# Kernel tuning notes

Measured on AMD Instinct MI355X. Metric: run time of the kernel, lower is better.

Reference implementation:

```python
import jax, jax.numpy as jnp
import numpy as np

N_NODES = 100000
N_EDGES = 1600000
IN_CH = 256
PROJ = 128
HID = 128
OUT = 32


def setup_inputs() -> dict:
    key = jax.random.key(0)
    ks = jax.random.split(key, 16)
    def lin(kw, kb, fan_in, fan_out):
        s = 1.0 / np.sqrt(fan_in)
        W = jax.random.uniform(kw, (fan_in, fan_out), jnp.float32, -s, s)
        b = jax.random.uniform(kb, (fan_out,), jnp.float32, -s, s)
        return W, b
    x = jax.random.normal(ks[0], (N_NODES, IN_CH), jnp.float32)
    edge_index = jax.random.randint(ks[1], (2, N_EDGES), 0, N_NODES, jnp.int32)
    edge_weight = jax.random.uniform(ks[2], (N_EDGES, 1), jnp.float32)
    Wp, bp = lin(ks[3], ks[4], IN_CH, PROJ)
    W1, b1 = lin(ks[5], ks[6], PROJ, HID)
    W2, b2 = lin(ks[7], ks[8], HID, HID)
    Wl1, bl1 = lin(ks[9], ks[10], HID, HID)
    Wl2, bl2 = lin(ks[11], ks[12], HID, OUT)
    return {"x": x, "edge_index": edge_index, "edge_weight": edge_weight,
            "Wp": Wp, "bp": bp, "W1": W1, "b1": b1, "W2": W2, "b2": b2,
            "Wl1": Wl1, "bl1": bl1, "Wl2": Wl2, "bl2": bl2}


def gcn_conv(x, W, b, src, dst, ew, n):
    # PyG GCNConv: add self-loops (weight 1), symmetric normalization.
    deg = jax.ops.segment_sum(ew, dst, num_segments=n) + 1.0  # self-loop adds 1
    dinv = jnp.where(deg > 0, jax.lax.rsqrt(deg), 0.0)        # [N]
    norm = dinv[src] * ew * dinv[dst]                          # [E]
    h = x @ W                                                  # [N, out]
    agg = jax.ops.segment_sum(norm[:, None] * h[src], dst, num_segments=n)
    agg = agg + (dinv * dinv)[:, None] * h                     # self-loop messages
    return agg + b


def reference(x, edge_index, edge_weight, Wp, bp, W1, b1, W2, b2, Wl1, bl1, Wl2, bl2):
    n = x.shape[0]
    src, dst = edge_index[0], edge_index[1]
    ew = edge_weight.squeeze(-1)
    h = jax.nn.relu(x @ Wp + bp)
    h = jax.nn.relu(gcn_conv(h, W1, b1, src, dst, ew, n))
    h = jax.nn.relu(gcn_conv(h, W2, b2, src, dst, ew, n))
    h = jax.nn.relu(h @ Wl1 + bl1)
    logits = h @ Wl2 + bl2
    return jax.nn.softmax(logits, axis=-1)
```

## Files before the change

kernel.cpp:

```cpp
#include <hip/hip_runtime.h>


typedef __attribute__((ext_vector_type(8))) short bf16x8;
typedef __attribute__((ext_vector_type(4))) short bf16x4;
typedef __attribute__((ext_vector_type(4))) float f32x4;

__device__ __forceinline__ void atomAddF(float* p, float v) {
    unsafeAtomicAdd(p, v);
}

__device__ __forceinline__ ushort bf16_rne(float x) {
    unsigned int u = __float_as_uint(x);
    return (ushort)((u + 0x7FFFu + ((u >> 16) & 1u)) >> 16);
}

__device__ __forceinline__ int swz(int row, int k) {
    return k ^ (((row >> 1) & 3) << 3);
}

__global__ void deg_cnt_kernel(const int* __restrict__ dst, const float* __restrict__ ew,
                               unsigned long long* __restrict__ packed, int E) {
    int e = blockIdx.x * blockDim.x + threadIdx.x;
    if (e < E) {
        int d = dst[e];
        unsigned int fx = __float2uint_rn(ew[e] * 16777216.0f);
        atomicAdd(&packed[d], (1ULL << 32) | (unsigned long long)fx);
    }
}

__global__ void dinv_kernel(const unsigned long long* __restrict__ packed,
                            float* __restrict__ dinv, int N) {
    int i = blockIdx.x * blockDim.x + threadIdx.x;
    if (i < N) {
        float deg = (float)(unsigned int)(packed[i] & 0xFFFFFFFFull) * (1.0f / 16777216.0f);
        dinv[i] = 1.0f / sqrtf(deg + 1.0f);
    }
}

__global__ __launch_bounds__(256) void scan_reduce(const unsigned long long* __restrict__ packed,
                                                   int* __restrict__ bsum, int M) {
    __shared__ int wsum[4];
    const int t = threadIdx.x;
    const int base = blockIdx.x * 2048 + t * 8;
    int s = 0;
#pragma unroll
    for (int j = 0; j < 8; j++) {
        int i = base + j;
        if (i < M) s += (int)(packed[i] >> 32);
    }
#pragma unroll
    for (int off = 1; off < 64; off <<= 1) s += __shfl_xor(s, off);
    if ((t & 63) == 0) wsum[t >> 6] = s;
    __syncthreads();
    if (t == 0) bsum[blockIdx.x] = wsum[0] + wsum[1] + wsum[2] + wsum[3];
}

__global__ void scan_bsum(int* __restrict__ bsum, int* __restrict__ rowptr_last, int nb) {
    const int lane = threadIdx.x;
    const int chunk = (nb + 63) / 64;
    const int b0 = lane * chunk;
    const int b1 = min(b0 + chunk, nb);
    int s = 0;
    for (int i = b0; i < b1; i++) s += bsum[i];
    int inc = s;
#pragma unroll
    for (int off = 1; off < 64; off <<= 1) {
        int u = __shfl_up(inc, off);
        if (lane >= off) inc += u;
    }
    int run = inc - s;
    for (int i = b0; i < b1; i++) {
        int v = bsum[i];
        bsum[i] = run;
        run += v;
    }
    if (lane == 63) *rowptr_last = inc;
}

__global__ __launch_bounds__(256) void scan_down(const unsigned long long* __restrict__ packed,
                                                 const int* __restrict__ bsum,
                                                 int* __restrict__ rowptr,
                                                 int* __restrict__ cur, int M) {
    __shared__ int wpre[4];
    const int t = threadIdx.x;
    const int lane = t & 63;
    const int w = t >> 6;
    const int base = blockIdx.x * 2048 + t * 8;
    int c[8];
    int s = 0;
#pragma unroll
    for (int j = 0; j < 8; j++) {
        int i = base + j;
        c[j] = (i < M) ? (int)(packed[i] >> 32) : 0;
        s += c[j];
    }
    int inc = s;
#pragma unroll
    for (int off = 1; off < 64; off <<= 1) {
        int u = __shfl_up(inc, off);
        if (lane >= off) inc += u;
    }
    if (lane == 63) wpre[w] = inc;
    __syncthreads();
    int woff = 0;
#pragma unroll
    for (int i = 0; i < 4; i++)
        if (i < w) woff += wpre[i];
    int run = bsum[blockIdx.x] + woff + (inc - s);
#pragma unroll
    for (int j = 0; j < 8; j++) {
        int i = base + j;
        if (i < M) {
            rowptr[i] = run;
            cur[i] = run;
            run += c[j];
        }
    }
}

__global__ void reorder_kernel(const int* __restrict__ src, const int* __restrict__ dst,
                               const float* __restrict__ ew, const float* __restrict__ dinv,
                               int* __restrict__ cur, int2* __restrict__ pairs, int E) {
    int e = blockIdx.x * blockDim.x + threadIdx.x;
    if (e < E) {
        int s = src[e], d = dst[e];
        float w = dinv[s] * ew[e] * dinv[d];
        int pos = atomicAdd(&cur[d], 1);
        pairs[pos] = make_int2(s, __float_as_int(w));
    }
}

__global__ __launch_bounds__(256) void gather_kernel(
    const int* __restrict__ rowptr, const int2* __restrict__ pairs,
    const float* __restrict__ dinv, const float* __restrict__ hW,
    float* __restrict__ agg, int M)
{
    int gid = blockIdx.x * blockDim.x + threadIdx.x;
    int n = gid >> 5;
    int c = (gid & 31) * 4;
    if (n >= M) return;
    int beg = rowptr[n], end = rowptr[n + 1];
    float di = dinv[n];
    float s = di * di;
    float4 v = *reinterpret_cast<const float4*>(&hW[(size_t)n * 128 + c]);
    float4 acc0 = make_float4(s * v.x, s * v.y, s * v.z, s * v.w);
    float4 acc1 = make_float4(0.f, 0.f, 0.f, 0.f);

    int e = beg;
    for (; e + 4 <= end; e += 4) {
        int2 p0 = pairs[e + 0];
        int2 p1 = pairs[e + 1];
        int2 p2 = pairs[e + 2];
        int2 p3 = pairs[e + 3];
        float4 h0 = *reinterpret_cast<const float4*>(&hW[(size_t)p0.x * 128 + c]);
        float4 h1 = *reinterpret_cast<const float4*>(&hW[(size_t)p1.x * 128 + c]);
        float4 h2 = *reinterpret_cast<const float4*>(&hW[(size_t)p2.x * 128 + c]);
        float4 h3 = *reinterpret_cast<const float4*>(&hW[(size_t)p3.x * 128 + c]);
        float w0 = __int_as_float(p0.y), w1 = __int_as_float(p1.y);
        float w2 = __int_as_float(p2.y), w3 = __int_as_float(p3.y);
        acc0.x = fmaf(w0, h0.x, acc0.x); acc0.y = fmaf(w0, h0.y, acc0.y);
        acc0.z = fmaf(w0, h0.z, acc0.z); acc0.w = fmaf(w0, h0.w, acc0.w);
        acc1.x = fmaf(w1, h1.x, acc1.x); acc1.y = fmaf(w1, h1.y, acc1.y);
        acc1.z = fmaf(w1, h1.z, acc1.z); acc1.w = fmaf(w1, h1.w, acc1.w);
        acc0.x = fmaf(w2, h2.x, acc0.x); acc0.y = fmaf(w2, h2.y, acc0.y);
        acc0.z = fmaf(w2, h2.z, acc0.z); acc0.w = fmaf(w2, h2.w, acc0.w);
        acc1.x = fmaf(w3, h3.x, acc1.x); acc1.y = fmaf(w3, h3.y, acc1.y);
        acc1.z = fmaf(w3, h3.z, acc1.z); acc1.w = fmaf(w3, h3.w, acc1.w);
    }
    for (; e < end; e++) {
        int2 p = pairs[e];
        float w = __int_as_float(p.y);
        float4 h = *reinterpret_cast<const float4*>(&hW[(size_t)p.x * 128 + c]);
        acc0.x = fmaf(w, h.x, acc0.x);
        acc0.y = fmaf(w, h.y, acc0.y);
        acc0.z = fmaf(w, h.z, acc0.z);
        acc0.w = fmaf(w, h.w, acc0.w);
    }
    acc0.x += acc1.x; acc0.y += acc1.y; acc0.z += acc1.z; acc0.w += acc1.w;
    *reinterpret_cast<float4*>(&agg[(size_t)n * 128 + c]) = acc0;
}

template<int K, bool IN_BR, bool OUT_BR>
__global__ __launch_bounds__(256) void gemm_mfma(
    const float* __restrict__ A, const float* __restrict__ W,
    const float* __restrict__ in_bias, const float* __restrict__ out_bias,
    float* __restrict__ C, int M)
{
    __shared__ ushort Ah[128][40], Al[128][40], Bh[128][40], Bl[128][40];

    const int tid = threadIdx.x;
    const int lane = tid & 63;
    const int wave = tid >> 6;
    const int wm = (wave >> 1) * 64;
    const int wn = (wave & 1) * 64;
    const int m0 = blockIdx.x * 128;

    f32x4 acc[4][4] = {};

    const int ar = tid >> 1;
    const int ak = (tid & 1) * 16;
    const int bn = (tid & 31) * 4;
    const int bk = (tid >> 5) * 4;

    const int fm = lane & 15;
    const int fk = (lane >> 4) * 8;

    for (int k0 = 0; k0 < K; k0 += 32) {
        __syncthreads();
        {
            const bool valid = (m0 + ar) < M;
            const float* srcp = &A[(size_t)(m0 + ar) * K + k0 + ak];
#pragma unroll
            for (int q = 0; q < 2; q++) {
                float vv[8];
                if (valid) {
                    *reinterpret_cast<float4*>(&vv[0]) = *reinterpret_cast<const float4*>(srcp + q * 8);
                    *reinterpret_cast<float4*>(&vv[4]) = *reinterpret_cast<const float4*>(srcp + q * 8 + 4);
                } else {
#pragma unroll
                    for (int j = 0; j < 8; j++) vv[j] = 0.f;
                }
                if (IN_BR) {
                    const float* bp_ = &in_bias[k0 + ak + q * 8];
#pragma unroll
                    for (int j = 0; j < 8; j++) vv[j] = fmaxf(vv[j] + bp_[j], 0.f);
                }
#pragma unroll
                for (int h = 0; h < 2; h++) {
                    ushort hh[4], ll[4];
#pragma unroll
                    for (int j = 0; j < 4; j++) {
                        float x = vv[h * 4 + j];
                        ushort hi = bf16_rne(x);
                        float fhi = __uint_as_float((unsigned int)hi << 16);
                        hh[j] = hi;
                        ll[j] = bf16_rne(x - fhi);
                    }
                    int col = swz(ar, ak + q * 8 + h * 4);
                    *reinterpret_cast<bf16x4*>(&Ah[ar][col]) = *reinterpret_cast<bf16x4*>(hh);
                    *reinterpret_cast<bf16x4*>(&Al[ar][col]) = *reinterpret_cast<bf16x4*>(ll);
                }
            }
        }
        {
            float rr[4][4];
#pragma unroll
            for (int i = 0; i < 4; i++)
                *reinterpret_cast<float4*>(rr[i]) =
                    *reinterpret_cast<const float4*>(&W[(size_t)(k0 + bk + i) * 128 + bn]);
#pragma unroll
            for (int j = 0; j < 4; j++) {
                ushort hh[4], ll[4];
#pragma unroll
                for (int i = 0; i < 4; i++) {
                    float x = rr[i][j];
                    ushort hi = bf16_rne(x);
                    float fhi = __uint_as_float((unsigned int)hi << 16);
                    hh[i] = hi;
                    ll[i] = bf16_rne(x - fhi);
                }
                int n = bn + j;
                int col = swz(n, bk);
                *reinterpret_cast<bf16x4*>(&Bh[n][col]) = *reinterpret_cast<bf16x4*>(hh);
                *reinterpret_cast<bf16x4*>(&Bl[n][col]) = *reinterpret_cast<bf16x4*>(ll);
            }
        }
        __syncthreads();

        bf16x8 ah[4], al[4], bh[4], bl[4];
#pragma unroll
        for (int t = 0; t < 4; t++) {
            int am = wm + t * 16 + fm;
            int ac = swz(am, fk);
            ah[t] = *reinterpret_cast<const bf16x8*>(&Ah[am][ac]);
            al[t] = *reinterpret_cast<const bf16x8*>(&Al[am][ac]);
            int nn = wn + t * 16 + fm;
            int bc = swz(nn, fk);
            bh[t] = *reinterpret_cast<const bf16x8*>(&Bh[nn][bc]);
            bl[t] = *reinterpret_cast<const bf16x8*>(&Bl[nn][bc]);
        }
#pragma unroll
        for (int i = 0; i < 4; i++)
#pragma unroll
            for (int j = 0; j < 4; j++) {
                acc[i][j] = __builtin_amdgcn_mfma_f32_16x16x32_bf16(ah[i], bh[j], acc[i][j], 0, 0, 0);
                acc[i][j] = __builtin_amdgcn_mfma_f32_16x16x32_bf16(ah[i], bl[j], acc[i][j], 0, 0, 0);
                acc[i][j] = __builtin_amdgcn_mfma_f32_16x16x32_bf16(al[i], bh[j], acc[i][j], 0, 0, 0);
            }
    }

#pragma unroll
    for (int i = 0; i < 4; i++) {
        int rbase = m0 + wm + i * 16 + (lane >> 4) * 4;
#pragma unroll
        for (int q = 0; q < 4; q++) {
            int r = rbase + q;
            if (r < M) {
#pragma unroll
                for (int j = 0; j < 4; j++) {
                    int cidx = wn + j * 16 + (lane & 15);
                    float v = acc[i][j][q];
                    if (OUT_BR) v = fmaxf(v + out_bias[cidx], 0.f);
                    C[(size_t)r * 128 + cidx] = v;
                }
            }
        }
    }
}

__global__ __launch_bounds__(256) void logits_kernel(
    const float* __restrict__ a, const float* __restrict__ Wl2,
    const float* __restrict__ bl2, float* __restrict__ out, int M)
{
    __shared__ float sW2[128 * 32];
    const int tid = threadIdx.x;
    for (int i = tid * 4; i < 128 * 32; i += 256 * 4)
        *reinterpret_cast<float4*>(&sW2[i]) = *reinterpret_cast<const float4*>(&Wl2[i]);
    __syncthreads();

    const int lane = tid & 63;
    const int half = lane >> 5;
    const int o = lane & 31;
    const int hw = tid >> 5;
    const float lb = bl2[o];
    const int nhw = gridDim.x * 8;

    for (int n = blockIdx.x * 8 + hw; n < M; n += nhw) {
        float4 af = *reinterpret_cast<const float4*>(&a[(size_t)n * 128 + o * 4]);
        float p = 0.f;
#pragma unroll
        for (int c = 0; c < 32; c++) {
            int srcl = (half << 5) + c;
            float v0 = __shfl(af.x, srcl);
            float v1 = __shfl(af.y, srcl);
            float v2 = __shfl(af.z, srcl);
            float v3 = __shfl(af.w, srcl);
            int k = c * 4;
            p = fmaf(v0, sW2[(k + 0) * 32 + o], p);
            p = fmaf(v1, sW2[(k + 1) * 32 + o], p);
            p = fmaf(v2, sW2[(k + 2) * 32 + o], p);
            p = fmaf(v3, sW2[(k + 3) * 32 + o], p);
        }
        float l = p + lb;
        float m = l;
#pragma unroll
        for (int s = 16; s >= 1; s >>= 1) m = fmaxf(m, __shfl_xor(m, s));
        float e = __expf(l - m);
        float ssum = e;
#pragma unroll
        for (int s = 16; s >= 1; s >>= 1) ssum += __shfl_xor(ssum, s);
        out[(size_t)n * 32 + o] = e / ssum;
    }
}

extern "C" void kernel_launch(void* const* d_in, const int* in_sizes, int n_in,
                              void* d_out, int out_size, void* d_ws, size_t ws_size,
                              hipStream_t stream) {
    const float* x   = (const float*)d_in[0];
    const int*   ei  = (const int*)d_in[1];
    const float* ew  = (const float*)d_in[2];
    const float* Wp  = (const float*)d_in[3];
    const float* bp  = (const float*)d_in[4];
    const float* W1  = (const float*)d_in[5];
    const float* b1  = (const float*)d_in[6];
    const float* W2  = (const float*)d_in[7];
    const float* b2  = (const float*)d_in[8];
    const float* Wl1 = (const float*)d_in[9];
    const float* bl1 = (const float*)d_in[10];
    const float* Wl2 = (const float*)d_in[11];
    const float* bl2 = (const float*)d_in[12];
    float* out = (float*)d_out;

    const int M = in_sizes[0] / 256;
    const int E = in_sizes[2];
    const int* srcp = ei;
    const int* dstp = ei + E;

    char* ws = (char*)d_ws;
    size_t off = 0;
    auto alloc = [&](size_t bytes) { void* p = ws + off; off = (off + bytes + 255) & ~(size_t)255; return p; };
    unsigned long long* packed = (unsigned long long*)alloc((size_t)M * 8);
    float* dinv   = (float*)alloc((size_t)M * 4);
    int*   rowptr = (int*)  alloc((size_t)(M + 1) * 4);
    int*   cur    = (int*)  alloc((size_t)M * 4);
    int*   bsum   = (int*)  alloc((size_t)4096 * 4);
    int2*  pairs  = (int2*) alloc((size_t)E * 8);
    float* bufA   = (float*)alloc((size_t)M * 128 * 4);
    float* bufB   = (float*)alloc((size_t)M * 128 * 4);

    const int ntiles = (M + 2047) / 2048;

    hipMemsetAsync(packed, 0, (size_t)M * 8, stream);
    deg_cnt_kernel<<<(E + 255) / 256, 256, 0, stream>>>(dstp, ew, packed, E);
    dinv_kernel<<<(M + 255) / 256, 256, 0, stream>>>(packed, dinv, M);
    scan_reduce<<<ntiles, 256, 0, stream>>>(packed, bsum, M);
    scan_bsum<<<1, 64, 0, stream>>>(bsum, rowptr + M, ntiles);
    scan_down<<<ntiles, 256, 0, stream>>>(packed, bsum, rowptr, cur, M);
    reorder_kernel<<<(E + 255) / 256, 256, 0, stream>>>(srcp, dstp, ew, dinv, cur, pairs, E);

    const int gblocks = (M + 127) / 128;
    const int hblocks = (int)(((size_t)M * 32 + 255) / 256);

    gemm_mfma<256, false, true><<<gblocks, 256, 0, stream>>>(x, Wp, nullptr, bp, bufA, M);

    gemm_mfma<128, false, false><<<gblocks, 256, 0, stream>>>(bufA, W1, nullptr, nullptr, bufB, M);
    gather_kernel<<<hblocks, 256, 0, stream>>>(rowptr, pairs, dinv, bufB, bufA, M);

    gemm_mfma<128, true, false><<<gblocks, 256, 0, stream>>>(bufA, W2, b1, nullptr, bufB, M);
    gather_kernel<<<hblocks, 256, 0, stream>>>(rowptr, pairs, dinv, bufB, bufA, M);

    gemm_mfma<128, true, true><<<gblocks, 256, 0, stream>>>(bufA, Wl1, b2, bl1, bufB, M);
    logits_kernel<<<1024, 256, 0, stream>>>(bufB, Wl2, bl2, out, M);
}
```

Baseline: 790.9 us.

## Pre-split activations and weights into bf16 hi/lo planes; drop reorder atomics

Activations between the GEMMs and gathers are now stored as bf16 hi/lo planes, which the producing kernels write directly. The gather kernel applies bias and ReLU and emits the planes itself, so the next GEMM loads ready bf16 data instead of converting fp32 per tile. Weights are split once by a new kernel rather than in every GEMM block. The CSR reorder uses per-edge ranks returned by the degree atomic, so the second atomic pass and the cur array are gone. The cost is a few extra small kernel launches and scattered 2-byte plane stores in the first GEMM's epilogue.

```diff
diff --git a/kernel.cpp b/kernel.cpp
--- a/kernel.cpp
+++ b/kernel.cpp
@@ -5,10 +5,6 @@
 typedef __attribute__((ext_vector_type(4))) short bf16x4;
 typedef __attribute__((ext_vector_type(4))) float f32x4;
 
-__device__ __forceinline__ void atomAddF(float* p, float v) {
-    unsafeAtomicAdd(p, v);
-}
-
 __device__ __forceinline__ ushort bf16_rne(float x) {
     unsigned int u = __float_as_uint(x);
     return (ushort)((u + 0x7FFFu + ((u >> 16) & 1u)) >> 16);
@@ -19,12 +15,14 @@
 }
 
 __global__ void deg_cnt_kernel(const int* __restrict__ dst, const float* __restrict__ ew,
-                               unsigned long long* __restrict__ packed, int E) {
+                               unsigned long long* __restrict__ packed,
+                               int* __restrict__ rank, int E) {
     int e = blockIdx.x * blockDim.x + threadIdx.x;
     if (e < E) {
         int d = dst[e];
         unsigned int fx = __float2uint_rn(ew[e] * 16777216.0f);
-        atomicAdd(&packed[d], (1ULL << 32) | (unsigned long long)fx);
+        unsigned long long old = atomicAdd(&packed[d], (1ULL << 32) | (unsigned long long)fx);
+        rank[e] = (int)(old >> 32);
     }
 }
 
@@ -79,8 +77,7 @@
 
 __global__ __launch_bounds__(256) void scan_down(const unsigned long long* __restrict__ packed,
                                                  const int* __restrict__ bsum,
-                                                 int* __restrict__ rowptr,
-                                                 int* __restrict__ cur, int M) {
+                                                 int* __restrict__ rowptr, int M) {
     __shared__ int wpre[4];
     const int t = threadIdx.x;
     const int lane = t & 63;
@@ -112,7 +109,6 @@
         int i = base + j;
         if (i < M) {
             rowptr[i] = run;
-            cur[i] = run;
             run += c[j];
         }
     }
@@ -120,20 +116,35 @@
 
 __global__ void reorder_kernel(const int* __restrict__ src, const int* __restrict__ dst,
                                const float* __restrict__ ew, const float* __restrict__ dinv,
-                               int* __restrict__ cur, int2* __restrict__ pairs, int E) {
+                               const int* __restrict__ rowptr, const int* __restrict__ rank,
+                               int2* __restrict__ pairs, int E) {
     int e = blockIdx.x * blockDim.x + threadIdx.x;
     if (e < E) {
         int s = src[e], d = dst[e];
         float w = dinv[s] * ew[e] * dinv[d];
-        int pos = atomicAdd(&cur[d], 1);
-        pairs[pos] = make_int2(s, __float_as_int(w));
+        pairs[rowptr[d] + rank[e]] = make_int2(s, __float_as_int(w));
+    }
+}
+
+__global__ void split_w_kernel(const float* __restrict__ W, ushort* __restrict__ ph,
+                               ushort* __restrict__ pl, int total, int Kdim) {
+    int id = blockIdx.x * blockDim.x + threadIdx.x;
+    if (id < total) {
+        int k = id >> 7;
+        int n = id & 127;
+        float x = W[id];
+        ushort hi = bf16_rne(x);
+        float fhi = __uint_as_float((unsigned int)hi << 16);
+        ph[n * Kdim + k] = hi;
+        pl[n * Kdim + k] = bf16_rne(x - fhi);
     }
 }
 
 __global__ __launch_bounds__(256) void gather_kernel(
     const int* __restrict__ rowptr, const int2* __restrict__ pairs,
     const float* __restrict__ dinv, const float* __restrict__ hW,
-    float* __restrict__ agg, int M)
+    const float* __restrict__ bias, ushort* __restrict__ ph,
+    ushort* __restrict__ pl, int M)
 {
     int gid = blockIdx.x * blockDim.x + threadIdx.x;
     int n = gid >> 5;
@@ -176,15 +187,32 @@
         acc0.z = fmaf(w, h.z, acc0.z);
         acc0.w = fmaf(w, h.w, acc0.w);
     }
-    acc0.x += acc1.x; acc0.y += acc1.y; acc0.z += acc1.z; acc0.w += acc1.w;
-    *reinterpret_cast<float4*>(&agg[(size_t)n * 128 + c]) = acc0;
-}
-
-template<int K, bool IN_BR, bool OUT_BR>
+    float4 b = *reinterpret_cast<const float4*>(&bias[c]);
+    float t0 = fmaxf(acc0.x + acc1.x + b.x, 0.f);
+    float t1 = fmaxf(acc0.y + acc1.y + b.y, 0.f);
+    float t2 = fmaxf(acc0.z + acc1.z + b.z, 0.f);
+    float t3 = fmaxf(acc0.w + acc1.w + b.w, 0.f);
+    ushort h4[4], l4[4];
+    float tt[4] = {t0, t1, t2, t3};
+#pragma unroll
+    for (int j = 0; j < 4; j++) {
+        ushort hi = bf16_rne(tt[j]);
+        float fhi = __uint_as_float((unsigned int)hi << 16);
+        h4[j] = hi;
+        l4[j] = bf16_rne(tt[j] - fhi);
+    }
+    *reinterpret_cast<bf16x4*>(&ph[(size_t)n * 128 + c]) = *reinterpret_cast<bf16x4*>(h4);
+    *reinterpret_cast<bf16x4*>(&pl[(size_t)n * 128 + c]) = *reinterpret_cast<bf16x4*>(l4);
+}
+
+template<int K, bool A_PRE, bool OUT_BR, bool OUT_PLANES>
 __global__ __launch_bounds__(256) void gemm_mfma(
-    const float* __restrict__ A, const float* __restrict__ W,
-    const float* __restrict__ in_bias, const float* __restrict__ out_bias,
-    float* __restrict__ C, int M)
+    const float* __restrict__ A,
+    const ushort* __restrict__ Ahp, const ushort* __restrict__ Alp,
+    const ushort* __restrict__ Bhp, const ushort* __restrict__ Blp,
+    const float* __restrict__ out_bias,
+    float* __restrict__ C, ushort* __restrict__ Chp, ushort* __restrict__ Clp,
+    int M)
 {
     __shared__ ushort Ah[128][40], Al[128][40], Bh[128][40], Bl[128][40];
 
@@ -197,19 +225,33 @@
 
     f32x4 acc[4][4] = {};
 
-    const int ar = tid >> 1;
-    const int ak = (tid & 1) * 16;
-    const int bn = (tid & 31) * 4;
-    const int bk = (tid >> 5) * 4;
+    const int sr = tid >> 1;
+    const int sk = (tid & 1) * 16;
 
     const int fm = lane & 15;
     const int fk = (lane >> 4) * 8;
 
     for (int k0 = 0; k0 < K; k0 += 32) {
         __syncthreads();
-        {
-            const bool valid = (m0 + ar) < M;
-            const float* srcp = &A[(size_t)(m0 + ar) * K + k0 + ak];
+        if (A_PRE) {
+            const bool valid = (m0 + sr) < M;
+            bf16x8 zero = {};
+            bf16x8 h0 = zero, h1 = zero, l0 = zero, l1 = zero;
+            if (valid) {
+                const ushort* ph = &Ahp[(size_t)(m0 + sr) * K + k0 + sk];
+                const ushort* pl = &Alp[(size_t)(m0 + sr) * K + k0 + sk];
+                h0 = *reinterpret_cast<const bf16x8*>(ph);
+                h1 = *reinterpret_cast<const bf16x8*>(ph + 8);
+                l0 = *reinterpret_cast<const bf16x8*>(pl);
+                l1 = *reinterpret_cast<const bf16x8*>(pl + 8);
+            }
+            *reinterpret_cast<bf16x8*>(&Ah[sr][swz(sr, sk)]) = h0;
+            *reinterpret_cast<bf16x8*>(&Ah[sr][swz(sr, sk + 8)]) = h1;
+            *reinterpret_cast<bf16x8*>(&Al[sr][swz(sr, sk)]) = l0;
+            *reinterpret_cast<bf16x8*>(&Al[sr][swz(sr, sk + 8)]) = l1;
+        } else {
+            const bool valid = (m0 + sr) < M;
+            const float* srcp = &A[(size_t)(m0 + sr) * K + k0 + sk];
 #pragma unroll
             for (int q = 0; q < 2; q++) {
                 float vv[8];
@@ -220,50 +262,26 @@
 #pragma unroll
                     for (int j = 0; j < 8; j++) vv[j] = 0.f;
                 }
-                if (IN_BR) {
-                    const float* bp_ = &in_bias[k0 + ak + q * 8];
-#pragma unroll
-                    for (int j = 0; j < 8; j++) vv[j] = fmaxf(vv[j] + bp_[j], 0.f);
+                ushort hh[8], ll[8];
+#pragma unroll
+                for (int j = 0; j < 8; j++) {
+                    ushort hi = bf16_rne(vv[j]);
+                    float fhi = __uint_as_float((unsigned int)hi << 16);
+                    hh[j] = hi;
+                    ll[j] = bf16_rne(vv[j] - fhi);
                 }
-#pragma unroll
-                for (int h = 0; h < 2; h++) {
-                    ushort hh[4], ll[4];
-#pragma unroll
-                    for (int j = 0; j < 4; j++) {
-                        float x = vv[h * 4 + j];
-                        ushort hi = bf16_rne(x);
-                        float fhi = __uint_as_float((unsigned int)hi << 16);
-                        hh[j] = hi;
-                        ll[j] = bf16_rne(x - fhi);
-                    }
-                    int col = swz(ar, ak + q * 8 + h * 4);
-                    *reinterpret_cast<bf16x4*>(&Ah[ar][col]) = *reinterpret_cast<bf16x4*>(hh);
-                    *reinterpret_cast<bf16x4*>(&Al[ar][col]) = *reinterpret_cast<bf16x4*>(ll);
-                }
+                int col = swz(sr, sk + q * 8);
+                *reinterpret_cast<bf16x8*>(&Ah[sr][col]) = *reinterpret_cast<bf16x8*>(hh);
+                *reinterpret_cast<bf16x8*>(&Al[sr][col]) = *reinterpret_cast<bf16x8*>(ll);
             }
         }
         {
-            float rr[4][4];
-#pragma unroll
-            for (int i = 0; i < 4; i++)
-                *reinterpret_cast<float4*>(rr[i]) =
-                    *reinterpret_cast<const float4*>(&W[(size_t)(k0 + bk + i) * 128 + bn]);
-#pragma unroll
-            for (int j = 0; j < 4; j++) {
-                ushort hh[4], ll[4];
-#pragma unroll
-                for (int i = 0; i < 4; i++) {
-                    float x = rr[i][j];
-                    ushort hi = bf16_rne(x);
-                    float fhi = __uint_as_float((unsigned int)hi << 16);
-                    hh[i] = hi;
-                    ll[i] = bf16_rne(x - fhi);
-                }
-                int n = bn + j;
-                int col = swz(n, bk);
-                *reinterpret_cast<bf16x4*>(&Bh[n][col]) = *reinterpret_cast<bf16x4*>(hh);
-                *reinterpret_cast<bf16x4*>(&Bl[n][col]) = *reinterpret_cast<bf16x4*>(ll);
-            }
+            const ushort* ph = &Bhp[(size_t)sr * K + k0 + sk];
+            const ushort* pl = &Blp[(size_t)sr * K + k0 + sk];
+            *reinterpret_cast<bf16x8*>(&Bh[sr][swz(sr, sk)]) = *reinterpret_cast<const bf16x8*>(ph);
+            *reinterpret_cast<bf16x8*>(&Bh[sr][swz(sr, sk + 8)]) = *reinterpret_cast<const bf16x8*>(ph + 8);
+            *reinterpret_cast<bf16x8*>(&Bl[sr][swz(sr, sk)]) = *reinterpret_cast<const bf16x8*>(pl);
+            *reinterpret_cast<bf16x8*>(&Bl[sr][swz(sr, sk + 8)]) = *reinterpret_cast<const bf16x8*>(pl + 8);
         }
         __syncthreads();
 
@@ -301,7 +319,14 @@
                     int cidx = wn + j * 16 + (lane & 15);
                     float v = acc[i][j][q];
                     if (OUT_BR) v = fmaxf(v + out_bias[cidx], 0.f);
-                    C[(size_t)r * 128 + cidx] = v;
+                    if (OUT_PLANES) {
+                        ushort hi = bf16_rne(v);
+                        float fhi = __uint_as_float((unsigned int)hi << 16);
+                        Chp[(size_t)r * 128 + cidx] = hi;
+                        Clp[(size_t)r * 128 + cidx] = bf16_rne(v - fhi);
+                    } else {
+                        C[(size_t)r * 128 + cidx] = v;
+                    }
                 }
             }
         }
@@ -380,35 +405,54 @@
     size_t off = 0;
     auto alloc = [&](size_t bytes) { void* p = ws + off; off = (off + bytes + 255) & ~(size_t)255; return p; };
     unsigned long long* packed = (unsigned long long*)alloc((size_t)M * 8);
-    float* dinv   = (float*)alloc((size_t)M * 4);
-    int*   rowptr = (int*)  alloc((size_t)(M + 1) * 4);
-    int*   cur    = (int*)  alloc((size_t)M * 4);
-    int*   bsum   = (int*)  alloc((size_t)4096 * 4);
-    int2*  pairs  = (int2*) alloc((size_t)E * 8);
-    float* bufA   = (float*)alloc((size_t)M * 128 * 4);
-    float* bufB   = (float*)alloc((size_t)M * 128 * 4);
+    float*  dinv   = (float*) alloc((size_t)M * 4);
+    int*    rowptr = (int*)   alloc((size_t)(M + 1) * 4);
+    int*    bsum   = (int*)   alloc((size_t)4096 * 4);
+    int2*   pairs  = (int2*)  alloc((size_t)E * 8);
+    ushort* PAh    = (ushort*)alloc((size_t)M * 128 * 2);
+    ushort* PAl    = (ushort*)alloc((size_t)M * 128 * 2);
+    float*  F      = (float*) alloc((size_t)M * 128 * 4);
+    ushort* WPh    = (ushort*)alloc((size_t)256 * 128 * 2);
+    ushort* WPl    = (ushort*)alloc((size_t)256 * 128 * 2);
+    ushort* W1h    = (ushort*)alloc((size_t)128 * 128 * 2);
+    ushort* W1l    = (ushort*)alloc((size_t)128 * 128 * 2);
+    ushort* W2h    = (ushort*)alloc((size_t)128 * 128 * 2);
+    ushort* W2l    = (ushort*)alloc((size_t)128 * 128 * 2);
+    ushort* WL1h   = (ushort*)alloc((size_t)128 * 128 * 2);
+    ushort* WL1l   = (ushort*)alloc((size_t)128 * 128 * 2);
+
+    int* rank = (int*)F;
 
     const int ntiles = (M + 2047) / 2048;
 
     hipMemsetAsync(packed, 0, (size_t)M * 8, stream);
-    deg_cnt_kernel<<<(E + 255) / 256, 256, 0, stream>>>(dstp, ew, packed, E);
+    deg_cnt_kernel<<<(E + 255) / 256, 256, 0, stream>>>(dstp, ew, packed, rank, E);
     dinv_kernel<<<(M + 255) / 256, 256, 0, stream>>>(packed, dinv, M);
     scan_reduce<<<ntiles, 256, 0, stream>>>(packed, bsum, M);
     scan_bsum<<<1, 64, 0, stream>>>(bsum, rowptr + M, ntiles);
-    scan_down<<<ntiles, 256, 0, stream>>>(packed, bsum, rowptr, cur, M);
-    reorder_kernel<<<(E + 255) / 256, 256, 0, stream>>>(srcp, dstp, ew, dinv, cur, pairs, E);
+    scan_down<<<ntiles, 256, 0, stream>>>(packed, bsum, rowptr, M);
+    reorder_kernel<<<(E + 255) / 256, 256, 0, stream>>>(srcp, dstp, ew, dinv, rowptr, rank, pairs, E);
+
+    split_w_kernel<<<128, 256, 0, stream>>>(Wp, WPh, WPl, 256 * 128, 256);
+    split_w_kernel<<<64, 256, 0, stream>>>(W1, W1h, W1l, 128 * 128, 128);
+    split_w_kernel<<<64, 256, 0, stream>>>(W2, W2h, W2l, 128 * 128, 128);
+    split_w_kernel<<<64, 256, 0, stream>>>(Wl1, WL1h, WL1l, 128 * 128, 128);
 
     const int gblocks = (M + 127) / 128;
     const int hblocks = (int)(((size_t)M * 32 + 255) / 256);
 
-    gemm_mfma<256, false, true><<<gblocks, 256, 0, stream>>>(x, Wp, nullptr, bp, bufA, M);
-
-    gemm_mfma<128, false, false><<<gblocks, 256, 0, stream>>>(bufA, W1, nullptr, nullptr, bufB, M);
-    gather_kernel<<<hblocks, 256, 0, stream>>>(rowptr, pairs, dinv, bufB, bufA, M);
-
-    gemm_mfma<128, true, false><<<gblocks, 256, 0, stream>>>(bufA, W2, b1, nullptr, bufB, M);
-    gather_kernel<<<hblocks, 256, 0, stream>>>(rowptr, pairs, dinv, bufB, bufA, M);
-
-    gemm_mfma<128, true, true><<<gblocks, 256, 0, stream>>>(bufA, Wl1, b2, bl1, bufB, M);
-    logits_kernel<<<1024, 256, 0, stream>>>(bufB, Wl2, bl2, out, M);
-}
+    gemm_mfma<256, false, true, true><<<gblocks, 256, 0, stream>>>(
+        x, nullptr, nullptr, WPh, WPl, bp, nullptr, PAh, PAl, M);
+
+    gemm_mfma<128, true, false, false><<<gblocks, 256, 0, stream>>>(
+        nullptr, PAh, PAl, W1h, W1l, nullptr, F, nullptr, nullptr, M);
+    gather_kernel<<<hblocks, 256, 0, stream>>>(rowptr, pairs, dinv, F, b1, PAh, PAl, M);
+
+    gemm_mfma<128, true, false, false><<<gblocks, 256, 0, stream>>>(
+        nullptr, PAh, PAl, W2h, W2l, nullptr, F, nullptr, nullptr, M);
+    gather_kernel<<<hblocks, 256, 0, stream>>>(rowptr, pairs, dinv, F, b2, PAh, PAl, M);
+
+    gemm_mfma<128, true, true, false><<<gblocks, 256, 0, stream>>>(
+        nullptr, PAh, PAl, WL1h, WL1l, bl1, F, nullptr, nullptr, M);
+    logits_kernel<<<1024, 256, 0, stream>>>(F, Wl2, bl2, out, M);
+}
```

After: 749.4 us. 5.3% less time.
